# Kernel tuning notes

Measured on AMD Instinct MI355X. Metric: run time of the kernel, lower is better.

The kernel has to match this reference:

```python
import jax, jax.numpy as jnp
from jax import lax
import numpy as np

B, C, H, W = 4, 64, 256, 256
OUT = 64


def setup_inputs() -> dict:
    key = jax.random.key(0)
    k1, k2, k3 = jax.random.split(key, 3)
    x = jax.random.normal(k1, (B, C, H, W), dtype=jnp.float32)
    # kaiming-ish init; offset conv scaled small so sampled offsets stay moderate
    w_off = jax.random.normal(k2, (18, C, 3, 3), dtype=jnp.float32) * 0.05
    b_off = jnp.zeros((18,), dtype=jnp.float32)
    w_def = jax.random.normal(k3, (OUT, C, 3, 3), dtype=jnp.float32) * (2.0 / (9 * C)) ** 0.5
    b_def = jnp.zeros((OUT,), dtype=jnp.float32)
    return {"x": x, "w_off": w_off, "b_off": b_off, "w_def": w_def, "b_def": b_def}


def _bilinear_sample(img, ys, xs):
    """img: [B,C,H,W]; ys,xs: [B,H,W] float sample coords. Zero padding outside."""
    y0 = jnp.floor(ys)
    x0 = jnp.floor(xs)
    ly = ys - y0  # [B,H,W]
    lx = xs - x0
    y0i = y0.astype(jnp.int32)
    x0i = x0.astype(jnp.int32)

    def corner(yi, xi):
        valid = (yi >= 0) & (yi < H) & (xi >= 0) & (xi < W)
        yc = jnp.clip(yi, 0, H - 1)
        xc = jnp.clip(xi, 0, W - 1)
        # gather per batch: [C,H,W] indexed by [H,W],[H,W] -> [C,H,W]
        v = jax.vmap(lambda im, a, b: im[:, a, b])(img, yc, xc)  # [B,C,H,W]
        return v * valid[:, None, :, :].astype(img.dtype)

    v00 = corner(y0i, x0i)
    v01 = corner(y0i, x0i + 1)
    v10 = corner(y0i + 1, x0i)
    v11 = corner(y0i + 1, x0i + 1)
    ly = ly[:, None, :, :]
    lx = lx[:, None, :, :]
    return (v00 * (1 - ly) * (1 - lx) + v01 * (1 - ly) * lx
            + v10 * ly * (1 - lx) + v11 * ly * lx)


def reference(x, w_off, b_off, w_def, b_def):
    # offset conv: 3x3, stride 1, pad 1 ('SAME')
    offsets = lax.conv_general_dilated(x, w_off, (1, 1), 'SAME') + b_off[None, :, None, None]
    offsets = offsets.reshape(B, 9, 2, H, W)  # per-tap (dy, dx), torchvision ordering

    hh = jnp.arange(H, dtype=x.dtype)[None, :, None]  # [1,H,1]
    ww = jnp.arange(W, dtype=x.dtype)[None, None, :]  # [1,1,W]

    out = jnp.zeros((B, OUT, H, W), dtype=x.dtype)
    for k in range(9):  # fixed small kernel loop
        ki, kj = k // 3, k % 3
        ys = hh + (ki - 1) + offsets[:, k, 0]  # pad=1 -> base = h + ki - 1
        xs = ww + (kj - 1) + offsets[:, k, 1]
        sampled = _bilinear_sample(x, ys, xs)  # [B,C,H,W]
        out = out + jnp.einsum('bchw,oc->bohw', sampled, w_def[:, :, ki, kj])
    return out + b_def[None, :, None, None]
```

## Files before the change

### kernel.cpp

```cpp
#include <hip/hip_runtime.h>


typedef _Float16 half8 __attribute__((ext_vector_type(8)));
typedef _Float16 h2    __attribute__((ext_vector_type(2)));
typedef float floatx4  __attribute__((ext_vector_type(4)));

namespace {
constexpr int B_ = 4, C_ = 64, H_ = 256, W_ = 256, OUT_ = 64;
constexpr int HW_ = H_ * W_;
constexpr size_t XT_BYTES = (size_t)B_ * HW_ * C_ * 2;
constexpr size_t WOFF_OFF = XT_BYTES;
constexpr int    WOFF_N   = 9 * 2 * 2 * 64 * 8;
constexpr size_t WDEF_OFF = WOFF_OFF + (size_t)WOFF_N * 2;
constexpr int    WDEF_N   = 9 * 2 * 4 * 64 * 8;
}

__global__ __launch_bounds__(256)
void transpose_x(const float* __restrict__ x, _Float16* __restrict__ xt,
                 const float* __restrict__ w_off, const float* __restrict__ w_def,
                 _Float16* __restrict__ wof, _Float16* __restrict__ wdf)
{
    __shared__ float tile[64 * 132];
    const int bid = blockIdx.x;
    const int half = bid & 1;
    const int row = bid >> 1;
    const int b = row >> 8, y = row & 255;
    const int t = threadIdx.x;
    const float* __restrict__ xp = x + (size_t)b * C_ * HW_ + y * W_ + half * 128;

#pragma unroll
    for (int i = 0; i < 8; ++i) {
        const int c = i * 8 + (t >> 5);
        const int px = (t & 31) * 4;
        const float4 v = *(const float4*)&xp[(size_t)c * HW_ + px];
        *(float4*)&tile[c * 132 + px] = v;
    }
    __syncthreads();

#pragma unroll
    for (int rr = 0; rr < 4; ++rr) {
        const int kcq = (t >> 7) * 4 + rr;
        const int px = t & 127;
        union { _Float16 h[8]; uint4 u; } g;
#pragma unroll
        for (int cc = 0; cc < 8; ++cc)
            g.h[cc] = (_Float16)tile[(kcq * 8 + cc) * 132 + px];
        *(uint4*)(xt + (((size_t)row * 8 + kcq) * 256 + half * 128 + px) * 8) = g.u;
    }

    if (bid < 32) {
        const int i0 = bid * 256 + threadIdx.x;
        for (int s = i0; s < OUT_ * C_ * 9; s += 8192) {
            const int n = s / 576;
            const int r = s - n * 576;
            const int c = r / 9;
            const int tap = r - c * 9;
            const int idx = ((((tap * 2 + (c >> 5)) * 4 + (n >> 4)) * 64
                              + ((c >> 3) & 3) * 16 + (n & 15)) << 3) + (c & 7);
            wdf[idx] = (_Float16)w_def[s];
        }
        for (int s = i0; s < 18 * C_ * 9; s += 8192) {
            const int n = s / 576;
            const int r = s - n * 576;
            const int c = r / 9;
            const int tap = r - c * 9;
            const int idx = ((((tap * 2 + (c >> 5)) * 2 + (n >> 4)) * 64
                              + ((c >> 3) & 3) * 16 + (n & 15)) << 3) + (c & 7);
            wof[idx] = (_Float16)w_off[s];
        }
        for (int i = i0; i < WOFF_N; i += 8192) {
            const int lane = (i >> 3) & 63, nt = (i >> 9) & 1;
            if (nt == 1 && (lane & 15) >= 2) wof[i] = (_Float16)0.0f;
        }
    }
}

__device__ __forceinline__ void bilin_setup(float ys, float xs, int* a, float* w)
{
    const float y0f = floorf(ys), x0f = floorf(xs);
    const float ly = ys - y0f, lx = xs - x0f;
    const int y0 = (int)y0f, x0 = (int)x0f;
    const int y1 = y0 + 1, x1 = x0 + 1;
    const int y0c = min(max(y0, 0), H_ - 1);
    const int y1c = min(max(y1, 0), H_ - 1);
    const int x0c = min(max(x0, 0), W_ - 1);
    const int x1c = min(max(x1, 0), W_ - 1);
    const float fy0 = (y0 >= 0 && y0 < H_) ? 1.0f : 0.0f;
    const float fy1 = (y1 >= 0 && y1 < H_) ? 1.0f : 0.0f;
    const float fx0 = (x0 >= 0 && x0 < W_) ? 1.0f : 0.0f;
    const float fx1 = (x1 >= 0 && x1 < W_) ? 1.0f : 0.0f;
    a[0] = y0c * 2048 + x0c;  w[0] = (1.0f - ly) * (1.0f - lx) * fy0 * fx0;
    a[1] = y0c * 2048 + x1c;  w[1] = (1.0f - ly) * lx          * fy0 * fx1;
    a[2] = y1c * 2048 + x0c;  w[2] = ly          * (1.0f - lx) * fy1 * fx0;
    a[3] = y1c * 2048 + x1c;  w[3] = ly          * lx          * fy1 * fx1;
}

__global__ __launch_bounds__(256, 2)
void deform_main(const _Float16* __restrict__ xt,
                 const _Float16* __restrict__ wof,
                 const float* __restrict__ b_off,
                 const _Float16* __restrict__ wdf,
                 const float* __restrict__ b_def,
                 float* __restrict__ out)
{
    __shared__ float off_lds[128 * 18];

    const int tid = threadIdx.x;
    const int lane = tid & 63;
    const int wv = tid >> 6;
    const int lm = lane & 15;
    const int lq = lane >> 4;
    const int bid = blockIdx.x;
    const int uid = (bid & 7) * 256 + (bid >> 3);
    const int colc = uid & 7;
    const int rowg = (uid >> 3) & 63;
    const int b = uid >> 9;
    const int y0 = rowg * 4;
    const int y = y0 + wv;
    const int base = colc * 32;
    const _Float16* __restrict__ xtb = xt + (size_t)b * HW_ * C_;

    {
        floatx4 acc1[2][2];
#pragma unroll
        for (int pt = 0; pt < 2; ++pt)
#pragma unroll
            for (int nt = 0; nt < 2; ++nt) acc1[pt][nt] = (floatx4)0.0f;

        uint4 st1[2][2];
        bool  v1[2][2];

#define P1_ISSUE(TAP, KC, PAR) do {                                          \
        const int dy_ = (TAP) / 3 - 1, dx_ = (TAP) % 3 - 1;                  \
        const int ys_ = y + dy_;                                             \
        const bool yok_ = (unsigned)ys_ < 256u;                              \
        const int ysc_ = min(max(ys_, 0), 255);                              \
        _Pragma("unroll")                                                    \
        for (int pt_ = 0; pt_ < 2; ++pt_) {                                  \
            const int pxs_ = base + pt_ * 16 + lm + dx_;                     \
            v1[PAR][pt_] = yok_ && ((unsigned)pxs_ < 256u);                  \
            const int pxc_ = min(max(pxs_, 0), 255);                         \
            st1[PAR][pt_] = *(const uint4*)(xtb +                            \
                (size_t)(ysc_ * 2048 + ((KC) * 4 + lq) * 256 + pxc_) * 8);   \
        } } while (0)

        P1_ISSUE(0, 0, 0);
        __builtin_amdgcn_sched_barrier(0);
#pragma unroll
        for (int g = 0; g < 18; ++g) {
            const int tap = g >> 1, kc = g & 1, par = g & 1;
            if (g < 17) {
                P1_ISSUE((g + 1) >> 1, (g + 1) & 1, (g + 1) & 1);
                __builtin_amdgcn_sched_barrier(0);
            }
            half8 bfr[2];
#pragma unroll
            for (int nt = 0; nt < 2; ++nt)
                bfr[nt] = *(const half8*)(wof +
                    ((size_t)(((tap * 2 + kc) * 2 + nt) * 64 + lane)) * 8);
#pragma unroll
            for (int pt = 0; pt < 2; ++pt) {
                uint4 t = st1[par][pt];
                if (!v1[par][pt]) { t.x = 0u; t.y = 0u; t.z = 0u; t.w = 0u; }
                const half8 afr = __builtin_bit_cast(half8, t);
#pragma unroll
                for (int nt = 0; nt < 2; ++nt)
                    acc1[pt][nt] = __builtin_amdgcn_mfma_f32_16x16x32_f16(
                        afr, bfr[nt], acc1[pt][nt], 0, 0, 0);
            }
        }
#undef P1_ISSUE

#pragma unroll
        for (int nt = 0; nt < 2; ++nt) {
            const int j = nt * 16 + lm;
            if (j < 18) {
                const float bj = b_off[j];
#pragma unroll
                for (int pt = 0; pt < 2; ++pt) {
#pragma unroll
                    for (int r = 0; r < 4; ++r) {
                        const int lpx = wv * 32 + pt * 16 + lq * 4 + r;
                        off_lds[lpx * 18 + j] = acc1[pt][nt][r] + bj;
                    }
                }
            }
        }
    }
    __syncthreads();

    floatx4 acc[2][4];
#pragma unroll
    for (int pt = 0; pt < 2; ++pt)
#pragma unroll
        for (int ot = 0; ot < 4; ++ot) acc[pt][ot] = (floatx4)0.0f;

    int   ca2[2][2][4];
    h2    cw2[2][2][4];
    uint4 stc[2][2][4];

#define P2_BILIN(TAP, TP) do {                                               \
        const int ki_ = (TAP) / 3, kj_ = (TAP) % 3;                          \
        _Pragma("unroll")                                                    \
        for (int pt_ = 0; pt_ < 2; ++pt_) {                                  \
            const int lpx_ = wv * 32 + pt_ * 16 + lm;                        \
            const float2 o2_ = *(const float2*)&off_lds[lpx_ * 18 + (TAP) * 2]; \
            const float ys_ = (float)(y + ki_ - 1) + o2_.x;                  \
            const float xs_ = (float)(base + pt_ * 16 + lm + kj_ - 1) + o2_.y; \
            float cwf_[4];                                                   \
            bilin_setup(ys_, xs_, ca2[TP][pt_], cwf_);                       \
            _Pragma("unroll")                                                \
            for (int c_ = 0; c_ < 4; ++c_)                                   \
                cw2[TP][pt_][c_] = (h2)((_Float16)cwf_[c_]);                 \
        } } while (0)

#define P2_ISSUE(TP, KC, PAR) do {                                           \
        const int plane_ = ((KC) * 4 + lq) * 256;                            \
        _Pragma("unroll")                                                    \
        for (int pt_ = 0; pt_ < 2; ++pt_)                                    \
            _Pragma("unroll")                                                \
            for (int c_ = 0; c_ < 4; ++c_)                                   \
                stc[PAR][pt_][c_] = *(const uint4*)(xtb +                    \
                    (size_t)(ca2[TP][pt_][c_] + plane_) * 8);                \
        } while (0)

    P2_BILIN(0, 0);
    P2_ISSUE(0, 0, 0);
    __builtin_amdgcn_sched_barrier(0);

#pragma unroll
    for (int g = 0; g < 18; ++g) {
        const int tap = g >> 1, kc = g & 1, par = g & 1, tp = (g >> 1) & 1;

        if (kc == 0) {
            P2_ISSUE(tp, 1, 1);
            __builtin_amdgcn_sched_barrier(0);
        } else if (tap < 8) {
            P2_ISSUE(tp ^ 1, 0, 0);
            __builtin_amdgcn_sched_barrier(0);
        }

        half8 bfr[4];
#pragma unroll
        for (int ot = 0; ot < 4; ++ot)
            bfr[ot] = *(const half8*)(wdf +
                ((size_t)(((tap * 2 + kc) * 4 + ot) * 64 + lane)) * 8);

        if (kc == 0 && tap < 8) P2_BILIN(tap + 1, tp ^ 1);

#pragma unroll
        for (int pt = 0; pt < 2; ++pt) {
            union Uc { uint4 u; h2 p[4]; } cc0, cc1, cc2, cc3;
            cc0.u = stc[par][pt][0];
            cc1.u = stc[par][pt][1];
            cc2.u = stc[par][pt][2];
            cc3.u = stc[par][pt][3];
            union Rr { h2 s[4]; half8 v; } r;
#pragma unroll
            for (int k = 0; k < 4; ++k)
                r.s[k] = cw2[tp][pt][0] * cc0.p[k] + cw2[tp][pt][1] * cc1.p[k]
                       + cw2[tp][pt][2] * cc2.p[k] + cw2[tp][pt][3] * cc3.p[k];
#pragma unroll
            for (int ot = 0; ot < 4; ++ot)
                acc[pt][ot] = __builtin_amdgcn_mfma_f32_16x16x32_f16(
                    r.v, bfr[ot], acc[pt][ot], 0, 0, 0);
        }
    }
#undef P2_BILIN
#undef P2_ISSUE

#pragma unroll
    for (int ot = 0; ot < 4; ++ot) {
        const int o = ot * 16 + lm;
        const float bd = b_def[o];
#pragma unroll
        for (int pt = 0; pt < 2; ++pt) {
            const int pxs = base + pt * 16 + lq * 4;
            const floatx4 a = acc[pt][ot];
            float4 v = make_float4(a[0] + bd, a[1] + bd, a[2] + bd, a[3] + bd);
            *(float4*)&out[(((size_t)b * OUT_ + o) * H_ + y) * W_ + pxs] = v;
        }
    }
}

extern "C" void kernel_launch(void* const* d_in, const int* in_sizes, int n_in,
                              void* d_out, int out_size, void* d_ws, size_t ws_size,
                              hipStream_t stream)
{
    const float* x     = (const float*)d_in[0];
    const float* w_off = (const float*)d_in[1];
    const float* b_off = (const float*)d_in[2];
    const float* w_def = (const float*)d_in[3];
    const float* b_def = (const float*)d_in[4];
    float* out = (float*)d_out;

    _Float16* xt  = (_Float16*)d_ws;
    _Float16* wof = (_Float16*)((char*)d_ws + WOFF_OFF);
    _Float16* wdf = (_Float16*)((char*)d_ws + WDEF_OFF);

    transpose_x<<<dim3(B_ * H_ * 2), dim3(256), 0, stream>>>(
        x, xt, w_off, w_def, wof, wdf);
    deform_main<<<dim3(B_ * H_ * 2), dim3(256), 0, stream>>>(
        xt, wof, b_off, wdf, b_def, out);
}
```

Baseline: 223.5 us.

## Split offset convolution into separate kernel and raise deform occupancy

Moves the 3x3 offset convolution out of deform_main into its own kernel that writes per-pixel offsets to a global workspace buffer. deform_main now just copies those offsets into LDS and its launch bound is raised from 2 to 4 blocks per SM. The goal is to cut register pressure in the main kernel and allow more waves in flight. The cost is an extra kernel launch and a global write and read of the offset tensor (about 19 MB), and the new conv kernel drops the software prefetch pipelining the fused version had.

Result: slower. 428.5 us (+91.7%).

```diff
diff --git a/kernel.cpp b/kernel.cpp
--- a/kernel.cpp
+++ b/kernel.cpp
@@ -13,6 +13,7 @@
 constexpr int    WOFF_N   = 9 * 2 * 2 * 64 * 8;
 constexpr size_t WDEF_OFF = WOFF_OFF + (size_t)WOFF_N * 2;
 constexpr int    WDEF_N   = 9 * 2 * 4 * 64 * 8;
+constexpr size_t OFFG_OFF = WDEF_OFF + (size_t)WDEF_N * 2;
 }
 
 __global__ __launch_bounds__(256)
@@ -71,6 +72,78 @@
         for (int i = i0; i < WOFF_N; i += 8192) {
             const int lane = (i >> 3) & 63, nt = (i >> 9) & 1;
             if (nt == 1 && (lane & 15) >= 2) wof[i] = (_Float16)0.0f;
+        }
+    }
+}
+
+__global__ __launch_bounds__(256)
+void offsets_conv(const _Float16* __restrict__ xt,
+                  const _Float16* __restrict__ wof,
+                  const float* __restrict__ b_off,
+                  float* __restrict__ off_g)
+{
+    const int tid = threadIdx.x;
+    const int lane = tid & 63;
+    const int wv = tid >> 6;
+    const int lm = lane & 15;
+    const int lq = lane >> 4;
+    const int bid = blockIdx.x;
+    const int half = bid & 1;
+    const int row = bid >> 1;
+    const int b = row >> 8, y = row & 255;
+    const int base = half * 128 + wv * 32;
+    const _Float16* __restrict__ xtb = xt + (size_t)b * HW_ * C_;
+
+    floatx4 acc1[2][2];
+#pragma unroll
+    for (int pt = 0; pt < 2; ++pt)
+#pragma unroll
+        for (int nt = 0; nt < 2; ++nt) acc1[pt][nt] = (floatx4)0.0f;
+
+#pragma unroll
+    for (int tap = 0; tap < 9; ++tap) {
+        const int dy = tap / 3 - 1, dx = tap % 3 - 1;
+        const int ys = y + dy;
+        const bool yok = (unsigned)ys < 256u;
+        const int ysc = min(max(ys, 0), 255);
+#pragma unroll
+        for (int kc = 0; kc < 2; ++kc) {
+            half8 bfr[2];
+#pragma unroll
+            for (int nt = 0; nt < 2; ++nt)
+                bfr[nt] = *(const half8*)(wof +
+                    ((size_t)(((tap * 2 + kc) * 2 + nt) * 64 + lane)) * 8);
+            const int plane = (kc * 4 + lq) * 256;
+#pragma unroll
+            for (int pt = 0; pt < 2; ++pt) {
+                const int px_s = base + pt * 16 + lm + dx;
+                const bool vld = yok && ((unsigned)px_s < 256u);
+                const int pxc = min(max(px_s, 0), 255);
+                uint4 t = *(const uint4*)(xtb +
+                    ((size_t)(ysc * 2048 + plane + pxc)) * 8);
+                if (!vld) { t.x = 0u; t.y = 0u; t.z = 0u; t.w = 0u; }
+                const half8 afr = __builtin_bit_cast(half8, t);
+#pragma unroll
+                for (int nt = 0; nt < 2; ++nt)
+                    acc1[pt][nt] = __builtin_amdgcn_mfma_f32_16x16x32_f16(
+                        afr, bfr[nt], acc1[pt][nt], 0, 0, 0);
+            }
+        }
+    }
+
+#pragma unroll
+    for (int nt = 0; nt < 2; ++nt) {
+        const int j = nt * 16 + lm;
+        if (j < 18) {
+            const float bj = b_off[j];
+#pragma unroll
+            for (int pt = 0; pt < 2; ++pt) {
+#pragma unroll
+                for (int r = 0; r < 4; ++r) {
+                    const int lpx = base + pt * 16 + lq * 4 + r;
+                    off_g[((size_t)row * 256 + lpx) * 18 + j] = acc1[pt][nt][r] + bj;
+                }
+            }
         }
     }
 }
@@ -95,10 +168,9 @@
     a[3] = y1c * 2048 + x1c;  w[3] = ly          * lx          * fy1 * fx1;
 }
 
-__global__ __launch_bounds__(256, 2)
+__global__ __launch_bounds__(256, 4)
 void deform_main(const _Float16* __restrict__ xt,
-                 const _Float16* __restrict__ wof,
-                 const float* __restrict__ b_off,
+                 const float* __restrict__ off_g,
                  const _Float16* __restrict__ wdf,
                  const float* __restrict__ b_def,
                  float* __restrict__ out)
@@ -121,71 +193,13 @@
     const _Float16* __restrict__ xtb = xt + (size_t)b * HW_ * C_;
 
     {
-        floatx4 acc1[2][2];
-#pragma unroll
-        for (int pt = 0; pt < 2; ++pt)
-#pragma unroll
-            for (int nt = 0; nt < 2; ++nt) acc1[pt][nt] = (floatx4)0.0f;
-
-        uint4 st1[2][2];
-        bool  v1[2][2];
-
-#define P1_ISSUE(TAP, KC, PAR) do {                                          \
-        const int dy_ = (TAP) / 3 - 1, dx_ = (TAP) % 3 - 1;                  \
-        const int ys_ = y + dy_;                                             \
-        const bool yok_ = (unsigned)ys_ < 256u;                              \
-        const int ysc_ = min(max(ys_, 0), 255);                              \
-        _Pragma("unroll")                                                    \
-        for (int pt_ = 0; pt_ < 2; ++pt_) {                                  \
-            const int pxs_ = base + pt_ * 16 + lm + dx_;                     \
-            v1[PAR][pt_] = yok_ && ((unsigned)pxs_ < 256u);                  \
-            const int pxc_ = min(max(pxs_, 0), 255);                         \
-            st1[PAR][pt_] = *(const uint4*)(xtb +                            \
-                (size_t)(ysc_ * 2048 + ((KC) * 4 + lq) * 256 + pxc_) * 8);   \
-        } } while (0)
-
-        P1_ISSUE(0, 0, 0);
-        __builtin_amdgcn_sched_barrier(0);
-#pragma unroll
-        for (int g = 0; g < 18; ++g) {
-            const int tap = g >> 1, kc = g & 1, par = g & 1;
-            if (g < 17) {
-                P1_ISSUE((g + 1) >> 1, (g + 1) & 1, (g + 1) & 1);
-                __builtin_amdgcn_sched_barrier(0);
-            }
-            half8 bfr[2];
-#pragma unroll
-            for (int nt = 0; nt < 2; ++nt)
-                bfr[nt] = *(const half8*)(wof +
-                    ((size_t)(((tap * 2 + kc) * 2 + nt) * 64 + lane)) * 8);
-#pragma unroll
-            for (int pt = 0; pt < 2; ++pt) {
-                uint4 t = st1[par][pt];
-                if (!v1[par][pt]) { t.x = 0u; t.y = 0u; t.z = 0u; t.w = 0u; }
-                const half8 afr = __builtin_bit_cast(half8, t);
-#pragma unroll
-                for (int nt = 0; nt < 2; ++nt)
-                    acc1[pt][nt] = __builtin_amdgcn_mfma_f32_16x16x32_f16(
-                        afr, bfr[nt], acc1[pt][nt], 0, 0, 0);
-            }
-        }
-#undef P1_ISSUE
-
-#pragma unroll
-        for (int nt = 0; nt < 2; ++nt) {
-            const int j = nt * 16 + lm;
-            if (j < 18) {
-                const float bj = b_off[j];
-#pragma unroll
-                for (int pt = 0; pt < 2; ++pt) {
-#pragma unroll
-                    for (int r = 0; r < 4; ++r) {
-                        const int lpx = wv * 32 + pt * 16 + lq * 4 + r;
-                        off_lds[lpx * 18 + j] = acc1[pt][nt][r] + bj;
-                    }
-                }
-            }
-        }
+        const int r = tid >> 6;
+        const int t64 = tid & 63;
+        const float* __restrict__ src =
+            off_g + ((size_t)(((b << 8) + y0 + r) * 256 + base)) * 18;
+#pragma unroll
+        for (int k = 0; k < 9; ++k)
+            off_lds[r * 576 + t64 * 9 + k] = src[t64 * 9 + k];
     }
     __syncthreads();
 
@@ -297,9 +311,12 @@
     _Float16* xt  = (_Float16*)d_ws;
     _Float16* wof = (_Float16*)((char*)d_ws + WOFF_OFF);
     _Float16* wdf = (_Float16*)((char*)d_ws + WDEF_OFF);
+    float*    offg = (float*)((char*)d_ws + OFFG_OFF);
 
     transpose_x<<<dim3(B_ * H_ * 2), dim3(256), 0, stream>>>(
         x, xt, w_off, w_def, wof, wdf);
+    offsets_conv<<<dim3(B_ * H_ * 2), dim3(256), 0, stream>>>(
+        xt, wof, b_off, offg);
     deform_main<<<dim3(B_ * H_ * 2), dim3(256), 0, stream>>>(
-        xt, wof, b_off, wdf, b_def, out);
-}
+        xt, offg, wdf, b_def, out);
+}
```
